# Kernel tuning notes

Measured on AMD Instinct MI355X. Metric: run time of the kernel, lower is better.

## Reference

```python
import jax, jax.numpy as jnp
import numpy as np

NUM_EXPERTS = 64
MODEL_DIM = 4096
NUM_TOKENS = 16384
TEMPERATURE = 1.0


def setup_inputs() -> dict:
    key = jax.random.key(0)
    kx, kw = jax.random.split(key)
    x = jax.random.normal(kx, (NUM_TOKENS, MODEL_DIM), dtype=jnp.float32)
    # gate weight: Linear(model_dim, num_experts, bias=False) -> W [E, D]
    W = jax.random.normal(kw, (NUM_EXPERTS, MODEL_DIM), dtype=jnp.float32) * 0.02
    return {"x": x, "W": W}


def reference(x, W):
    # logits = wg(x): [T, E]
    logits = jnp.einsum("td,ed->te", x, W)
    # use_fp32 path: logits already fp32
    gates = jax.nn.softmax(logits / TEMPERATURE, axis=1)  # [T, E]
    # top-1 (k=1 topk == argmax + gather)
    top1_idx = jnp.argmax(gates, axis=1)                   # [T]
    top1_p = jnp.take_along_axis(gates, top1_idx[:, None], axis=1)[:, 0]  # [T]
    # one-hot scatter of top1 prob, then permute(1,0) -> [E, T]
    mask1 = jax.nn.one_hot(top1_idx, NUM_EXPERTS, dtype=gates.dtype)      # [T, E]
    combine_weights = (mask1 * top1_p[:, None]).T                          # [E, T]
    # auxiliary load-balancing loss (indices1_s == top1_idx since argmax of gates)
    me = jnp.mean(gates, axis=0)   # [E]
    ce = jnp.mean(mask1, axis=0)   # [E]
    l_aux = jnp.mean(me * ce) * (NUM_EXPERTS * NUM_EXPERTS)
    return (l_aux, combine_weights)
```

## Files before the change

### kernel.cpp

```cpp
#include <hip/hip_runtime.h>
#include <hip/hip_bf16.h>

#define NTOK   16384
#define DIM    4096
#define NEXP   64
#define KSPLIT 8
#define KLEN   (DIM / KSPLIT)
#define BM     256
#define KSTEP  32
#define SMBLK  256

typedef __attribute__((ext_vector_type(8))) short bf16x8;
typedef __attribute__((ext_vector_type(4))) float f32x4;

__device__ __forceinline__ unsigned short f2bf(float f) {
    unsigned u = __float_as_uint(f);
    u += 0x7fffu + ((u >> 16) & 1u);
    return (unsigned short)(u >> 16);
}
__device__ __forceinline__ float bf2f(unsigned short h) {
    return __uint_as_float((unsigned)h << 16);
}

__global__ __launch_bounds__(256) void wsplit(const float* __restrict__ W,
                                              unsigned short* __restrict__ Wf) {
    const int s    = blockIdx.x * 256 + threadIdx.x;
    const int lane = s & 63;
    const int eb   = (s >> 6) & 3;
    const int kb   = s >> 8;
    const int e    = eb * 16 + (lane & 15);
    const int k8   = kb * 4 + (lane >> 4);

    const float4 w0 = *(const float4*)(W + (size_t)e * DIM + k8 * 8);
    const float4 w1 = *(const float4*)(W + (size_t)e * DIM + k8 * 8 + 4);
    float f[8] = {w0.x, w0.y, w0.z, w0.w, w1.x, w1.y, w1.z, w1.w};

    unsigned short hi[8], lo[8];
#pragma unroll
    for (int j = 0; j < 8; ++j) {
        hi[j] = f2bf(f[j]);
        lo[j] = f2bf(f[j] - bf2f(hi[j]));
    }
    const size_t fbase = ((size_t)(kb * 4 + eb) * 2) * 512;
    ushort4* ph = (ushort4*)(Wf + fbase + lane * 8);
    ushort4* pl = (ushort4*)(Wf + fbase + 512 + lane * 8);
    ph[0] = make_ushort4(hi[0], hi[1], hi[2], hi[3]);
    ph[1] = make_ushort4(hi[4], hi[5], hi[6], hi[7]);
    pl[0] = make_ushort4(lo[0], lo[1], lo[2], lo[3]);
    pl[1] = make_ushort4(lo[4], lo[5], lo[6], lo[7]);
}

__global__ __launch_bounds__(256, 2) void gate_gemm(const float* __restrict__ x,
                                                    const unsigned short* __restrict__ Wf,
                                                    float* __restrict__ part) {
    __shared__ float xt[BM * KSTEP];

    const int tid  = threadIdx.x;
    const int lane = tid & 63;
    const int wv   = tid >> 6;
    const int tb   = blockIdx.x & 63;
    const int ks   = blockIdx.x >> 6;
    const int k0   = ks * KLEN;

    const int g = lane >> 3;
    const int c = lane & 7;
    const int tw = wv * 64;

    float4 st[8];
#pragma unroll
    for (int i = 0; i < 8; ++i)
        st[i] = *(const float4*)(x + (size_t)(tb * BM + tw + i * 8 + g) * DIM + k0 + c * 4);

    f32x4 acc[4][4];
#pragma unroll
    for (int f = 0; f < 4; ++f)
#pragma unroll
        for (int eb = 0; eb < 4; ++eb) acc[f][eb] = (f32x4){0.f, 0.f, 0.f, 0.f};

    for (int kk = 0; kk < KLEN; kk += KSTEP) {
#pragma unroll
        for (int i = 0; i < 8; ++i) {
            const int t = tw + i * 8 + g;
            *(float4*)&xt[(size_t)t * KSTEP + ((c ^ g) * 4)] = st[i];
        }
        __syncthreads();

        if (kk + KSTEP < KLEN) {
#pragma unroll
            for (int i = 0; i < 8; ++i)
                st[i] = *(const float4*)(x + (size_t)(tb * BM + tw + i * 8 + g) * DIM
                                         + k0 + kk + KSTEP + c * 4);
        }

        const int kb = (k0 + kk) >> 5;
        bf16x8 bh[4], bl[4];
#pragma unroll
        for (int eb = 0; eb < 4; ++eb) {
            const size_t fbase = ((size_t)(kb * 4 + eb) * 2) * 512;
            bh[eb] = *(const bf16x8*)(Wf + fbase + lane * 8);
            bl[eb] = *(const bf16x8*)(Wf + fbase + 512 + lane * 8);
        }

#pragma unroll
        for (int f = 0; f < 4; ++f) {
            const int tf = tw + f * 16 + (lane & 15);
            const int c2 = (lane >> 4) * 2;
            const int t7 = tf & 7;
            const float4 xa = *(const float4*)&xt[(size_t)tf * KSTEP + ((c2 ^ t7) * 4)];
            const float4 xb = *(const float4*)&xt[(size_t)tf * KSTEP + (((c2 + 1) ^ t7) * 4)];
            float fv[8] = {xa.x, xa.y, xa.z, xa.w, xb.x, xb.y, xb.z, xb.w};
            bf16x8 ah, al;
#pragma unroll
            for (int j = 0; j < 8; ++j) {
                const __hip_bfloat16 h = __float2bfloat16(fv[j]);
                const __hip_bfloat16 l = __float2bfloat16(fv[j] - __bfloat162float(h));
                ah[j] = *(const short*)&h;
                al[j] = *(const short*)&l;
            }
#pragma unroll
            for (int eb = 0; eb < 4; ++eb) {
                acc[f][eb] = __builtin_amdgcn_mfma_f32_16x16x32_bf16(ah, bh[eb], acc[f][eb], 0, 0, 0);
                acc[f][eb] = __builtin_amdgcn_mfma_f32_16x16x32_bf16(ah, bl[eb], acc[f][eb], 0, 0, 0);
                acc[f][eb] = __builtin_amdgcn_mfma_f32_16x16x32_bf16(al, bh[eb], acc[f][eb], 0, 0, 0);
            }
        }
        __syncthreads();
    }

    const int r0 = (lane >> 4) * 4;
#pragma unroll
    for (int f = 0; f < 4; ++f) {
        float* p = part + ((size_t)ks * NTOK + tb * BM + tw + f * 16 + r0) * NEXP + (lane & 15);
#pragma unroll
        for (int eb = 0; eb < 4; ++eb)
#pragma unroll
            for (int r = 0; r < 4; ++r)
                p[(size_t)r * NEXP + eb * 16] = acc[f][eb][r];
    }
}

__global__ __launch_bounds__(256) void gate_softmax(const float* __restrict__ part,
                                                    float* __restrict__ out,
                                                    float* __restrict__ gSp,
                                                    float* __restrict__ gCp) {
    __shared__ float smS[NEXP];
    __shared__ float smC[NEXP];
    const int tid = threadIdx.x;
    if (tid < NEXP) { smS[tid] = 0.f; smC[tid] = 0.f; }
    __syncthreads();

    const int lane = tid & 63;
    const int wid  = blockIdx.x * 4 + (tid >> 6);
    const int TPW  = NTOK / (SMBLK * 4);

    float meacc = 0.f, ceacc = 0.f;

    for (int i = 0; i < TPW; ++i) {
        const int t = wid * TPW + i;
        float logit = 0.f;
#pragma unroll
        for (int ks = 0; ks < KSPLIT; ++ks)
            logit += part[((size_t)ks * NTOK + t) * NEXP + lane];

        float m = logit; int mi = lane;
#pragma unroll
        for (int off = 32; off; off >>= 1) {
            float om = __shfl_xor(m, off);
            int   oi = __shfl_xor(mi, off);
            if (om > m || (om == m && oi < mi)) { m = om; mi = oi; }
        }
        const float ex = __expf(logit - m);
        float s = ex;
#pragma unroll
        for (int off = 32; off; off >>= 1) s += __shfl_xor(s, off);

        meacc += ex / s;
        if (lane == mi) {
            ceacc += 1.f;
            out[1 + (size_t)lane * NTOK + t] = 1.f / s;
        }
    }

    atomicAdd(&smS[lane], meacc);
    atomicAdd(&smC[lane], ceacc);
    __syncthreads();
    if (tid < NEXP) {
        gSp[blockIdx.x * NEXP + tid] = smS[tid];
        gCp[blockIdx.x * NEXP + tid] = smC[tid];
    }
}

__global__ __launch_bounds__(1024) void gate_laux(const float* __restrict__ gSp,
                                                  const float* __restrict__ gCp,
                                                  float* __restrict__ out) {
    __shared__ float sS[NEXP];
    __shared__ float sC[NEXP];
    const int tid = threadIdx.x;
    if (tid < NEXP) { sS[tid] = 0.f; sC[tid] = 0.f; }
    __syncthreads();

    float accS = 0.f, accC = 0.f;
    for (int i = tid; i < SMBLK * NEXP; i += 1024) {
        accS += gSp[i];
        accC += gCp[i];
    }
    atomicAdd(&sS[tid & 63], accS);
    atomicAdd(&sC[tid & 63], accC);
    __syncthreads();

    if (tid < NEXP) {
        float v = sS[tid] * sC[tid];
#pragma unroll
        for (int off = 32; off; off >>= 1) v += __shfl_xor(v, off);
        if (tid == 0)
            out[0] = v * (float)NEXP / ((float)NTOK * (float)NTOK);
    }
}

extern "C" void kernel_launch(void* const* d_in, const int* in_sizes, int n_in,
                              void* d_out, int out_size, void* d_ws, size_t ws_size,
                              hipStream_t stream) {
    const float* x = (const float*)d_in[0];
    const float* W = (const float*)d_in[1];
    float* out = (float*)d_out;

    char* base = (char*)d_ws;
    float*          gSp  = (float*)base;
    float*          gCp  = (float*)(base + (size_t)SMBLK * NEXP * 4);
    unsigned short* Wf   = (unsigned short*)(base + 2 * (size_t)SMBLK * NEXP * 4);
    float*          part = (float*)(base + 2 * (size_t)SMBLK * NEXP * 4
                                    + (size_t)128 * 4 * 2 * 512 * 2);

    hipMemsetAsync(d_out, 0, (size_t)out_size * sizeof(float), stream);

    wsplit<<<dim3(128), 256, 0, stream>>>(W, Wf);
    gate_gemm<<<dim3(64 * KSPLIT), 256, 0, stream>>>(x, Wf, part);
    gate_softmax<<<dim3(SMBLK), 256, 0, stream>>>(part, out, gSp, gCp);
    gate_laux<<<dim3(1), 1024, 0, stream>>>(gSp, gCp, out);
}
```

Baseline: 437.1 us.

## Fuse gate GEMM with softmax/top-1 epilogue using in-block two-way K split

Replaces the 8-way split-K GEMM and separate softmax kernel with one fused kernel. Each 512-thread block handles 64 tokens, with two wave groups each covering half of K, reducing their partials through LDS. The block then computes softmax, argmax and the combine weights directly from the MFMA accumulators. This removes the partial-logit workspace round trip and one launch. Each wave now stages its own x tile in per-wave LDS without block barriers and reads W fragments directly each step. The trade-offs are less parallelism per token and a longer per-block K loop.

```diff
diff --git a/kernel.cpp b/kernel.cpp
--- a/kernel.cpp
+++ b/kernel.cpp
@@ -4,11 +4,10 @@
 #define NTOK   16384
 #define DIM    4096
 #define NEXP   64
-#define KSPLIT 8
-#define KLEN   (DIM / KSPLIT)
-#define BM     256
 #define KSTEP  32
-#define SMBLK  256
+#define KHALF  2048
+#define ITERS  (KHALF / KSTEP)
+#define NBLK   256
 
 typedef __attribute__((ext_vector_type(8))) short bf16x8;
 typedef __attribute__((ext_vector_type(4))) float f32x4;
@@ -50,143 +49,142 @@
     pl[1] = make_ushort4(lo[4], lo[5], lo[6], lo[7]);
 }
 
-__global__ __launch_bounds__(256, 2) void gate_gemm(const float* __restrict__ x,
-                                                    const unsigned short* __restrict__ Wf,
-                                                    float* __restrict__ part) {
-    __shared__ float xt[BM * KSTEP];
+__global__ __launch_bounds__(512, 2) void gate_fused(const float* __restrict__ x,
+                                                     const unsigned short* __restrict__ Wf,
+                                                     float* __restrict__ out,
+                                                     float* __restrict__ gSp,
+                                                     float* __restrict__ gCp) {
+    __shared__ float ldsx[8][2][16][32];
+    __shared__ f32x4 red[4][4][64];
+    __shared__ float smS[NEXP];
+    __shared__ float smC[NEXP];
 
     const int tid  = threadIdx.x;
     const int lane = tid & 63;
     const int wv   = tid >> 6;
-    const int tb   = blockIdx.x & 63;
-    const int ks   = blockIdx.x >> 6;
-    const int k0   = ks * KLEN;
-
-    const int g = lane >> 3;
-    const int c = lane & 7;
-    const int tw = wv * 64;
-
-    float4 st[8];
-#pragma unroll
-    for (int i = 0; i < 8; ++i)
-        st[i] = *(const float4*)(x + (size_t)(tb * BM + tw + i * 8 + g) * DIM + k0 + c * 4);
-
-    f32x4 acc[4][4];
-#pragma unroll
-    for (int f = 0; f < 4; ++f)
-#pragma unroll
-        for (int eb = 0; eb < 4; ++eb) acc[f][eb] = (f32x4){0.f, 0.f, 0.f, 0.f};
-
-    for (int kk = 0; kk < KLEN; kk += KSTEP) {
-#pragma unroll
-        for (int i = 0; i < 8; ++i) {
-            const int t = tw + i * 8 + g;
-            *(float4*)&xt[(size_t)t * KSTEP + ((c ^ g) * 4)] = st[i];
-        }
-        __syncthreads();
-
-        if (kk + KSTEP < KLEN) {
-#pragma unroll
-            for (int i = 0; i < 8; ++i)
-                st[i] = *(const float4*)(x + (size_t)(tb * BM + tw + i * 8 + g) * DIM
-                                         + k0 + kk + KSTEP + c * 4);
-        }
-
-        const int kb = (k0 + kk) >> 5;
-        bf16x8 bh[4], bl[4];
+    const int wq   = wv & 3;
+    const int kw   = wv >> 2;
+    const int tb   = blockIdx.x;
+    const int tq   = tb * 64 + wq * 16;
+
+    if (tid < NEXP) { smS[tid] = 0.f; smC[tid] = 0.f; }
+
+    const int tokrow = lane >> 2;
+    const int c0     = lane & 3;
+    const int rs     = tokrow & 7;
+    const int cw0    = (c0 ^ rs) * 4;
+    const int cw1    = ((c0 + 4) ^ rs) * 4;
+    const float* xpre = x + (size_t)(tq + tokrow) * DIM + kw * KHALF + c0 * 4;
+
+    const int tfr = lane & 15;
+    const int rs2 = tfr & 7;
+    const int c2  = (lane >> 4) * 2;
+    const int ra  = (c2 ^ rs2) * 4;
+    const int rb  = ((c2 + 1) ^ rs2) * 4;
+    const int kbase = kw * ITERS;
+
+    f32x4 acc[4];
+#pragma unroll
+    for (int eb = 0; eb < 4; ++eb) acc[eb] = (f32x4){0.f, 0.f, 0.f, 0.f};
+
+    auto body = [&](float4& A, float4& B, int itc, int buf) {
+        *(float4*)&ldsx[wv][buf][tokrow][cw0] = A;
+        *(float4*)&ldsx[wv][buf][tokrow][cw1] = B;
+        if (itc + 4 < ITERS) {
+            A = *(const float4*)(xpre + (size_t)(itc + 4) * KSTEP);
+            B = *(const float4*)(xpre + (size_t)(itc + 4) * KSTEP + 16);
+        }
+        const float4 xa = *(const float4*)&ldsx[wv][buf][tfr][ra];
+        const float4 xb = *(const float4*)&ldsx[wv][buf][tfr][rb];
+        const float fv[8] = {xa.x, xa.y, xa.z, xa.w, xb.x, xb.y, xb.z, xb.w};
+        bf16x8 ah, al;
+#pragma unroll
+        for (int j = 0; j < 8; ++j) {
+            const __hip_bfloat16 h = __float2bfloat16(fv[j]);
+            const __hip_bfloat16 l = __float2bfloat16(fv[j] - __bfloat162float(h));
+            ah[j] = *(const short*)&h;
+            al[j] = *(const short*)&l;
+        }
+        const int kbv = kbase + itc;
 #pragma unroll
         for (int eb = 0; eb < 4; ++eb) {
-            const size_t fbase = ((size_t)(kb * 4 + eb) * 2) * 512;
-            bh[eb] = *(const bf16x8*)(Wf + fbase + lane * 8);
-            bl[eb] = *(const bf16x8*)(Wf + fbase + 512 + lane * 8);
-        }
-
-#pragma unroll
-        for (int f = 0; f < 4; ++f) {
-            const int tf = tw + f * 16 + (lane & 15);
-            const int c2 = (lane >> 4) * 2;
-            const int t7 = tf & 7;
-            const float4 xa = *(const float4*)&xt[(size_t)tf * KSTEP + ((c2 ^ t7) * 4)];
-            const float4 xb = *(const float4*)&xt[(size_t)tf * KSTEP + (((c2 + 1) ^ t7) * 4)];
-            float fv[8] = {xa.x, xa.y, xa.z, xa.w, xb.x, xb.y, xb.z, xb.w};
-            bf16x8 ah, al;
-#pragma unroll
-            for (int j = 0; j < 8; ++j) {
-                const __hip_bfloat16 h = __float2bfloat16(fv[j]);
-                const __hip_bfloat16 l = __float2bfloat16(fv[j] - __bfloat162float(h));
-                ah[j] = *(const short*)&h;
-                al[j] = *(const short*)&l;
+            const size_t fbase = ((size_t)(kbv * 4 + eb) * 2) * 512;
+            const bf16x8 bh = *(const bf16x8*)(Wf + fbase + lane * 8);
+            const bf16x8 bl = *(const bf16x8*)(Wf + fbase + 512 + lane * 8);
+            acc[eb] = __builtin_amdgcn_mfma_f32_16x16x32_bf16(ah, bh, acc[eb], 0, 0, 0);
+            acc[eb] = __builtin_amdgcn_mfma_f32_16x16x32_bf16(ah, bl, acc[eb], 0, 0, 0);
+            acc[eb] = __builtin_amdgcn_mfma_f32_16x16x32_bf16(al, bh, acc[eb], 0, 0, 0);
+        }
+    };
+
+    float4 s0a = *(const float4*)(xpre + 0 * KSTEP), s0b = *(const float4*)(xpre + 0 * KSTEP + 16);
+    float4 s1a = *(const float4*)(xpre + 1 * KSTEP), s1b = *(const float4*)(xpre + 1 * KSTEP + 16);
+    float4 s2a = *(const float4*)(xpre + 2 * KSTEP), s2b = *(const float4*)(xpre + 2 * KSTEP + 16);
+    float4 s3a = *(const float4*)(xpre + 3 * KSTEP), s3b = *(const float4*)(xpre + 3 * KSTEP + 16);
+
+    for (int it = 0; it < ITERS; it += 4) {
+        body(s0a, s0b, it + 0, 0);
+        body(s1a, s1b, it + 1, 1);
+        body(s2a, s2b, it + 2, 0);
+        body(s3a, s3b, it + 3, 1);
+    }
+
+    __syncthreads();
+    if (kw == 1) {
+#pragma unroll
+        for (int eb = 0; eb < 4; ++eb) red[wq][eb][lane] = acc[eb];
+    }
+    __syncthreads();
+
+    if (kw == 0) {
+#pragma unroll
+        for (int eb = 0; eb < 4; ++eb) acc[eb] += red[wq][eb][lane];
+
+        const int col = lane & 15;
+        const int G   = lane >> 4;
+        float me0 = 0.f, me1 = 0.f, me2 = 0.f, me3 = 0.f;
+        float ce0 = 0.f, ce1 = 0.f, ce2 = 0.f, ce3 = 0.f;
+
+#pragma unroll
+        for (int r = 0; r < 4; ++r) {
+            float m = acc[0][r]; int me = col;
+            if (acc[1][r] > m) { m = acc[1][r]; me = 16 + col; }
+            if (acc[2][r] > m) { m = acc[2][r]; me = 32 + col; }
+            if (acc[3][r] > m) { m = acc[3][r]; me = 48 + col; }
+#pragma unroll
+            for (int mask = 1; mask <= 8; mask <<= 1) {
+                const float om = __shfl_xor(m, mask);
+                const int   oe = __shfl_xor(me, mask);
+                if (om > m || (om == m && oe < me)) { m = om; me = oe; }
             }
-#pragma unroll
-            for (int eb = 0; eb < 4; ++eb) {
-                acc[f][eb] = __builtin_amdgcn_mfma_f32_16x16x32_bf16(ah, bh[eb], acc[f][eb], 0, 0, 0);
-                acc[f][eb] = __builtin_amdgcn_mfma_f32_16x16x32_bf16(ah, bl[eb], acc[f][eb], 0, 0, 0);
-                acc[f][eb] = __builtin_amdgcn_mfma_f32_16x16x32_bf16(al, bh[eb], acc[f][eb], 0, 0, 0);
+            const float e0 = __expf(acc[0][r] - m);
+            const float e1 = __expf(acc[1][r] - m);
+            const float e2 = __expf(acc[2][r] - m);
+            const float e3 = __expf(acc[3][r] - m);
+            float s = e0 + e1 + e2 + e3;
+#pragma unroll
+            for (int mask = 1; mask <= 8; mask <<= 1) s += __shfl_xor(s, mask);
+            const float inv = 1.f / s;
+            me0 += e0 * inv; me1 += e1 * inv; me2 += e2 * inv; me3 += e3 * inv;
+
+            if (col == (me & 15)) {
+                const int tok = tq + G * 4 + r;
+                out[1 + (size_t)me * NTOK + tok] = inv;
+                ce0 += (me >> 4) == 0 ? 1.f : 0.f;
+                ce1 += (me >> 4) == 1 ? 1.f : 0.f;
+                ce2 += (me >> 4) == 2 ? 1.f : 0.f;
+                ce3 += (me >> 4) == 3 ? 1.f : 0.f;
             }
         }
-        __syncthreads();
-    }
-
-    const int r0 = (lane >> 4) * 4;
-#pragma unroll
-    for (int f = 0; f < 4; ++f) {
-        float* p = part + ((size_t)ks * NTOK + tb * BM + tw + f * 16 + r0) * NEXP + (lane & 15);
-#pragma unroll
-        for (int eb = 0; eb < 4; ++eb)
-#pragma unroll
-            for (int r = 0; r < 4; ++r)
-                p[(size_t)r * NEXP + eb * 16] = acc[f][eb][r];
-    }
-}
-
-__global__ __launch_bounds__(256) void gate_softmax(const float* __restrict__ part,
-                                                    float* __restrict__ out,
-                                                    float* __restrict__ gSp,
-                                                    float* __restrict__ gCp) {
-    __shared__ float smS[NEXP];
-    __shared__ float smC[NEXP];
-    const int tid = threadIdx.x;
-    if (tid < NEXP) { smS[tid] = 0.f; smC[tid] = 0.f; }
-    __syncthreads();
-
-    const int lane = tid & 63;
-    const int wid  = blockIdx.x * 4 + (tid >> 6);
-    const int TPW  = NTOK / (SMBLK * 4);
-
-    float meacc = 0.f, ceacc = 0.f;
-
-    for (int i = 0; i < TPW; ++i) {
-        const int t = wid * TPW + i;
-        float logit = 0.f;
-#pragma unroll
-        for (int ks = 0; ks < KSPLIT; ++ks)
-            logit += part[((size_t)ks * NTOK + t) * NEXP + lane];
-
-        float m = logit; int mi = lane;
-#pragma unroll
-        for (int off = 32; off; off >>= 1) {
-            float om = __shfl_xor(m, off);
-            int   oi = __shfl_xor(mi, off);
-            if (om > m || (om == m && oi < mi)) { m = om; mi = oi; }
-        }
-        const float ex = __expf(logit - m);
-        float s = ex;
-#pragma unroll
-        for (int off = 32; off; off >>= 1) s += __shfl_xor(s, off);
-
-        meacc += ex / s;
-        if (lane == mi) {
-            ceacc += 1.f;
-            out[1 + (size_t)lane * NTOK + t] = 1.f / s;
-        }
-    }
-
-    atomicAdd(&smS[lane], meacc);
-    atomicAdd(&smC[lane], ceacc);
+        atomicAdd(&smS[col],      me0); atomicAdd(&smS[16 + col], me1);
+        atomicAdd(&smS[32 + col], me2); atomicAdd(&smS[48 + col], me3);
+        atomicAdd(&smC[col],      ce0); atomicAdd(&smC[16 + col], ce1);
+        atomicAdd(&smC[32 + col], ce2); atomicAdd(&smC[48 + col], ce3);
+    }
     __syncthreads();
     if (tid < NEXP) {
-        gSp[blockIdx.x * NEXP + tid] = smS[tid];
-        gCp[blockIdx.x * NEXP + tid] = smC[tid];
+        gSp[(size_t)tb * NEXP + tid] = smS[tid];
+        gCp[(size_t)tb * NEXP + tid] = smC[tid];
     }
 }
 
@@ -200,7 +198,7 @@
     __syncthreads();
 
     float accS = 0.f, accC = 0.f;
-    for (int i = tid; i < SMBLK * NEXP; i += 1024) {
+    for (int i = tid; i < NBLK * NEXP; i += 1024) {
         accS += gSp[i];
         accC += gCp[i];
     }
@@ -225,16 +223,13 @@
     float* out = (float*)d_out;
 
     char* base = (char*)d_ws;
-    float*          gSp  = (float*)base;
-    float*          gCp  = (float*)(base + (size_t)SMBLK * NEXP * 4);
-    unsigned short* Wf   = (unsigned short*)(base + 2 * (size_t)SMBLK * NEXP * 4);
-    float*          part = (float*)(base + 2 * (size_t)SMBLK * NEXP * 4
-                                    + (size_t)128 * 4 * 2 * 512 * 2);
+    float*          gSp = (float*)base;
+    float*          gCp = (float*)(base + (size_t)NBLK * NEXP * 4);
+    unsigned short* Wf  = (unsigned short*)(base + 2 * (size_t)NBLK * NEXP * 4);
 
     hipMemsetAsync(d_out, 0, (size_t)out_size * sizeof(float), stream);
 
     wsplit<<<dim3(128), 256, 0, stream>>>(W, Wf);
-    gate_gemm<<<dim3(64 * KSPLIT), 256, 0, stream>>>(x, Wf, part);
-    gate_softmax<<<dim3(SMBLK), 256, 0, stream>>>(part, out, gSp, gCp);
+    gate_fused<<<dim3(NBLK), 512, 0, stream>>>(x, Wf, out, gSp, gCp);
     gate_laux<<<dim3(1), 1024, 0, stream>>>(gSp, gCp, out);
 }
```

Result: faster. 411.1 us (-5.9%).
